# Optimization experiments

Measured on AMD Instinct MI355X. Metric: run time of the kernel, lower is better.

## Reference

```python
import jax, jax.numpy as jnp
import numpy as np
from jax.ops import segment_sum

IN_DIM, HID_DIM, OUT_DIM = 128, 128, 64
N_NODES, N_EDGES = 50000, 800000


def gcn_conv(x, src, dst, W, b, n_nodes):
    # Symmetric GCN normalization (no self loops): deg at targets from unit weights
    deg = segment_sum(jnp.ones(src.shape[0], dtype=x.dtype), dst, num_segments=n_nodes)
    dinv = jnp.where(deg > 0, jax.lax.rsqrt(jnp.maximum(deg, 1.0)), 0.0)
    norm = dinv[src] * dinv[dst]                      # [E]
    h = x @ W                                         # [N, out] small GEMM first (PyG order)
    msg = h[src] * norm[:, None]                      # gather + scale: [E, out]
    out = segment_sum(msg, dst, num_segments=n_nodes) # scatter-add to targets
    return out + b


def setup_inputs() -> dict:
    key = jax.random.key(0)
    k1, k2, k3, k4, k5 = jax.random.split(key, 5)
    x = jax.random.normal(k1, (N_NODES, IN_DIM), dtype=jnp.float32)
    edge_index = jax.random.randint(k2, (2, N_EDGES), 0, N_NODES, dtype=jnp.int64)
    s1 = 1.0 / np.sqrt(IN_DIM)
    s2 = 1.0 / np.sqrt(HID_DIM)
    W1 = jax.random.uniform(k3, (IN_DIM, HID_DIM), jnp.float32, -s1, s1)
    b1 = jnp.zeros((HID_DIM,), jnp.float32)
    W2 = jax.random.uniform(k4, (HID_DIM, OUT_DIM), jnp.float32, -s2, s2)
    b2 = jnp.zeros((OUT_DIM,), jnp.float32)
    return {"x": x, "edge_index": edge_index, "W1": W1, "b1": b1, "W2": W2, "b2": b2}


def reference(x, edge_index, W1, b1, W2, b2):
    n_nodes = x.shape[0]
    src, dst = edge_index[0], edge_index[1]
    h = gcn_conv(x, src, dst, W1, b1, n_nodes)
    h = jax.nn.relu(h)
    # Dropout is identity in eval mode (reference is deterministic)
    out = gcn_conv(h, src, dst, W2, b2, n_nodes)
    return out
```

## Files before the change

kernel.cpp:

```cpp
#include <hip/hip_runtime.h>

#define N_NODES 50000
#define N_EDGES 800000
#define IN_DIM  128
#define HID_DIM 128
#define OUT_DIM 64

#define NPAD 50176
#define CAP  64
#define GEMM1B ((N_NODES + 63) / 64)
#define FILLB (N_EDGES / 256)
#define W2PREPB 8

typedef __attribute__((ext_vector_type(8))) short bf16x8;
typedef __attribute__((ext_vector_type(4))) float f32x4;
typedef __attribute__((ext_vector_type(2))) float f32x2;

__device__ __forceinline__ unsigned short f2bf(float f) {
    unsigned u = __float_as_uint(f);
    u += 0x7fffu + ((u >> 16) & 1u);
    return (unsigned short)(u >> 16);
}
__device__ __forceinline__ float bflo(unsigned u) { return __uint_as_float(u << 16); }
__device__ __forceinline__ float bfhi(unsigned u) { return __uint_as_float(u & 0xffff0000u); }

#define ACC8(u)  do { \
    acc[0] += bflo(u.x); acc[1] += bfhi(u.x); \
    acc[2] += bflo(u.y); acc[3] += bfhi(u.y); \
    acc[4] += bflo(u.z); acc[5] += bfhi(u.z); \
    acc[6] += bflo(u.w); acc[7] += bfhi(u.w); } while (0)

__device__ __forceinline__ unsigned char f2fp8(float f) {
    return (unsigned char)(__builtin_amdgcn_cvt_pk_fp8_f32(f, f, 0, false) & 0xff);
}

#define ACCF8(u)  do { \
    f32x2 p0 = __builtin_amdgcn_cvt_pk_f32_fp8((int)u.x, false); \
    f32x2 p1 = __builtin_amdgcn_cvt_pk_f32_fp8((int)u.x, true);  \
    f32x2 p2 = __builtin_amdgcn_cvt_pk_f32_fp8((int)u.y, false); \
    f32x2 p3 = __builtin_amdgcn_cvt_pk_f32_fp8((int)u.y, true);  \
    acc[0] += p0[0]; acc[1] += p0[1]; \
    acc[2] += p1[0]; acc[3] += p1[1]; \
    acc[4] += p2[0]; acc[5] += p2[1]; \
    acc[6] += p3[0]; acc[7] += p3[1]; } while (0)

__device__ __forceinline__ float deg2dinv(int deg) {
    return (deg > 0) ? rsqrtf((float)deg) : 0.0f;
}

#define W1T_STRIDE 136


__global__ __launch_bounds__(256) void prep_fill_kernel(const int* __restrict__ src,
                                                        const int* __restrict__ dst,
                                                        int* __restrict__ cnt,
                                                        unsigned short* __restrict__ csr_src,
                                                        const float* __restrict__ W2,
                                                        unsigned short* __restrict__ w2t) {
    int bid = blockIdx.x;
    int tid = threadIdx.x;
    if (bid < W2PREPB) {
        int idx = bid * 256 + tid;
        int c = idx >> 5, k4 = (idx & 31) * 4;
        ushort4 o;
        o.x = f2bf(W2[(k4 + 0) * 64 + c]);
        o.y = f2bf(W2[(k4 + 1) * 64 + c]);
        o.z = f2bf(W2[(k4 + 2) * 64 + c]);
        o.w = f2bf(W2[(k4 + 3) * 64 + c]);
        *(ushort4*)(w2t + c * 128 + k4) = o;
    } else {
        int e = (bid - W2PREPB) * 256 + tid;
        int s = src[e], d = dst[e];
        int slot = atomicAdd(&cnt[d], 1);
        if (slot < CAP) csr_src[(d << 6) + slot] = (unsigned short)s;
    }
}


__global__ __launch_bounds__(256) void gemm1_kernel(const float* __restrict__ x,
                                                    const float* __restrict__ W1,
                                                    const int* __restrict__ cnt,
                                                    unsigned char* __restrict__ h1f8) {
    __shared__ unsigned short w1t[128 * W1T_STRIDE];

    int tid = threadIdx.x;
#pragma unroll
    for (int i = 0; i < 64; ++i) {
        int idx = i * 256 + tid;
        int k = idx >> 7, c = idx & 127;
        w1t[c * W1T_STRIDE + k] = f2bf(W1[idx]);
    }
    __syncthreads();

    int wave = tid >> 6;
    int lane = tid & 63;
    int n = lane & 15, quad = lane >> 4;
    int row0 = blockIdx.x * 64 + wave * 16;

    int arow = row0 + n;
    if (arow >= N_NODES) arow = N_NODES - 1;
    const float* aptr = x + (size_t)arow * 128 + quad * 8;
    const unsigned short* bbase = w1t + (size_t)n * W1T_STRIDE + quad * 8;

    f32x4 acc[8];
#pragma unroll
    for (int t = 0; t < 8; ++t) acc[t] = (f32x4){0.f, 0.f, 0.f, 0.f};

#pragma unroll
    for (int w4 = 0; w4 < 4; ++w4) {
        float4 f0 = *(const float4*)(aptr + w4 * 32);
        float4 f1 = *(const float4*)(aptr + w4 * 32 + 4);
        bf16x8 af;
        af[0] = (short)f2bf(f0.x); af[1] = (short)f2bf(f0.y);
        af[2] = (short)f2bf(f0.z); af[3] = (short)f2bf(f0.w);
        af[4] = (short)f2bf(f1.x); af[5] = (short)f2bf(f1.y);
        af[6] = (short)f2bf(f1.z); af[7] = (short)f2bf(f1.w);
#pragma unroll
        for (int t = 0; t < 8; ++t) {
            bf16x8 bf = *(const bf16x8*)(bbase + (size_t)t * 16 * W1T_STRIDE + w4 * 32);
            acc[t] = __builtin_amdgcn_mfma_f32_16x16x32_bf16(af, bf, acc[t], 0, 0, 0);
        }
    }

#pragma unroll
    for (int r = 0; r < 4; ++r) {
        int row = row0 + quad * 4 + r;
        if (row < N_NODES) {
            float dn = deg2dinv(cnt[row]);
            unsigned char* o = h1f8 + (size_t)row * 128 + n;
#pragma unroll
            for (int t = 0; t < 8; ++t) o[t * 16] = f2fp8(acc[t][r] * dn);
        }
    }
}


#define A1T_STRIDE 136

__global__ __launch_bounds__(256) void agg1_gemm2_fused(const unsigned short* __restrict__ csr_src,
                                                        const int* __restrict__ cnt,
                                                        const float* __restrict__ b1,
                                                        const unsigned char* __restrict__ h1f8,
                                                        const unsigned short* __restrict__ w2t,
                                                        unsigned short* __restrict__ h2b) {
    __shared__ unsigned short a1t[16 * A1T_STRIDE];

    int node0 = blockIdx.x * 16;
    int g = threadIdx.x >> 4;
    int q = threadIdx.x & 15;
    int node = node0 + g;
    int start = node << 6;
    int m = cnt[node];
    float dn = deg2dinv(m);
    if (m > CAP) m = CAP;

    float acc[8] = {};
    int j = 0;
    for (; j + 7 < m; j += 8) {
        ushort4 sa = *(const ushort4*)(csr_src + start + j);
        ushort4 sb = *(const ushort4*)(csr_src + start + j + 4);
        uint2 u0 = ((const uint2*)(h1f8 + (size_t)sa.x * 128))[q];
        uint2 u1 = ((const uint2*)(h1f8 + (size_t)sa.y * 128))[q];
        uint2 u2 = ((const uint2*)(h1f8 + (size_t)sa.z * 128))[q];
        uint2 u3 = ((const uint2*)(h1f8 + (size_t)sa.w * 128))[q];
        uint2 u4 = ((const uint2*)(h1f8 + (size_t)sb.x * 128))[q];
        uint2 u5 = ((const uint2*)(h1f8 + (size_t)sb.y * 128))[q];
        uint2 u6 = ((const uint2*)(h1f8 + (size_t)sb.z * 128))[q];
        uint2 u7 = ((const uint2*)(h1f8 + (size_t)sb.w * 128))[q];
        ACCF8(u0); ACCF8(u1); ACCF8(u2); ACCF8(u3);
        ACCF8(u4); ACCF8(u5); ACCF8(u6); ACCF8(u7);
    }
    for (; j + 3 < m; j += 4) {
        ushort4 sa = *(const ushort4*)(csr_src + start + j);
        uint2 u0 = ((const uint2*)(h1f8 + (size_t)sa.x * 128))[q];
        uint2 u1 = ((const uint2*)(h1f8 + (size_t)sa.y * 128))[q];
        uint2 u2 = ((const uint2*)(h1f8 + (size_t)sa.z * 128))[q];
        uint2 u3 = ((const uint2*)(h1f8 + (size_t)sa.w * 128))[q];
        ACCF8(u0); ACCF8(u1); ACCF8(u2); ACCF8(u3);
    }
    for (; j < m; ++j) {
        int s0 = csr_src[start + j];
        uint2 u0 = ((const uint2*)(h1f8 + (size_t)s0 * 128))[q];
        ACCF8(u0);
    }

    {
        float4 bA = ((const float4*)b1)[2 * q];
        float4 bB = ((const float4*)b1)[2 * q + 1];
        ushort4 oA, oB;
        oA.x = f2bf(fmaxf(acc[0] * dn + bA.x, 0.f));
        oA.y = f2bf(fmaxf(acc[1] * dn + bA.y, 0.f));
        oA.z = f2bf(fmaxf(acc[2] * dn + bA.z, 0.f));
        oA.w = f2bf(fmaxf(acc[3] * dn + bA.w, 0.f));
        oB.x = f2bf(fmaxf(acc[4] * dn + bB.x, 0.f));
        oB.y = f2bf(fmaxf(acc[5] * dn + bB.y, 0.f));
        oB.z = f2bf(fmaxf(acc[6] * dn + bB.z, 0.f));
        oB.w = f2bf(fmaxf(acc[7] * dn + bB.w, 0.f));
        ushort4* o = (ushort4*)(a1t + g * A1T_STRIDE + q * 8);
        o[0] = oA;
        o[1] = oB;
    }
    __syncthreads();

    int wave = threadIdx.x >> 6;
    int lane = threadIdx.x & 63;
    int n = lane & 15, quad = lane >> 4;
    const unsigned short* bbase = w2t + (size_t)(wave * 16 + n) * 128 + quad * 8;
    const unsigned short* abase = a1t + (size_t)n * A1T_STRIDE + quad * 8;

    f32x4 c2 = (f32x4){0.f, 0.f, 0.f, 0.f};
#pragma unroll
    for (int w4 = 0; w4 < 4; ++w4) {
        bf16x8 af = *(const bf16x8*)(abase + w4 * 32);
        bf16x8 bf = *(const bf16x8*)(bbase + w4 * 32);
        c2 = __builtin_amdgcn_mfma_f32_16x16x32_bf16(af, bf, c2, 0, 0, 0);
    }

#pragma unroll
    for (int r = 0; r < 4; ++r) {
        int row = node0 + quad * 4 + r;
        float dr = deg2dinv(cnt[row]);
        h2b[(size_t)row * 64 + wave * 16 + n] = f2bf(c2[r] * dr);
    }
}


__global__ __launch_bounds__(256) void agg2_kernel(const unsigned short* __restrict__ csr_src,
                                                   const int* __restrict__ cnt,
                                                   const float* __restrict__ b2,
                                                   const unsigned short* __restrict__ h2b,
                                                   float* __restrict__ out) {
    int node = blockIdx.x * 4 + (threadIdx.x >> 6);
    if (node >= N_NODES) return;
    int lane = threadIdx.x & 63;
    int grp = lane >> 3;
    int q   = lane & 7;
    int start = node << 6;
    int m = cnt[node];
    float dn = deg2dinv(m);
    if (m > CAP) m = CAP;

    float acc[8] = {};

    int j = grp;
    for (; j + 8 < m; j += 16) {
        int s0 = csr_src[start + j];
        int s1 = csr_src[start + j + 8];
        uint4 u0 = ((const uint4*)(h2b + (size_t)s0 * 64))[q];
        uint4 u1 = ((const uint4*)(h2b + (size_t)s1 * 64))[q];
        ACC8(u0); ACC8(u1);
    }
    if (j < m) {
        int s0 = csr_src[start + j];
        uint4 u0 = ((const uint4*)(h2b + (size_t)s0 * 64))[q];
        ACC8(u0);
    }

#pragma unroll
    for (int d = 8; d <= 32; d <<= 1) {
#pragma unroll
        for (int c = 0; c < 8; ++c) acc[c] += __shfl_xor(acc[c], d, 64);
    }

    if (lane < 8) {
        float4 bA = ((const float4*)b2)[2 * q];
        float4 bB = ((const float4*)b2)[2 * q + 1];
        float4 rA, rB;
        rA.x = acc[0] * dn + bA.x;
        rA.y = acc[1] * dn + bA.y;
        rA.z = acc[2] * dn + bA.z;
        rA.w = acc[3] * dn + bA.w;
        rB.x = acc[4] * dn + bB.x;
        rB.y = acc[5] * dn + bB.y;
        rB.z = acc[6] * dn + bB.z;
        rB.w = acc[7] * dn + bB.w;
        float4* o = (float4*)(out + (size_t)node * 64);
        o[2 * q] = rA;
        o[2 * q + 1] = rB;
    }
}


extern "C" void kernel_launch(void* const* d_in, const int* in_sizes, int n_in,
                              void* d_out, int out_size, void* d_ws, size_t ws_size,
                              hipStream_t stream) {
    const float* x  = (const float*)d_in[0];
    const int*   ei = (const int*)d_in[1];
    const float* W1 = (const float*)d_in[2];
    const float* b1 = (const float*)d_in[3];
    const float* W2 = (const float*)d_in[4];
    const float* b2 = (const float*)d_in[5];
    float* out = (float*)d_out;

    const int* src = ei;
    const int* dst = ei + N_EDGES;

    char* ws = (char*)d_ws;
    int*   cnt       = (int*)ws;
    unsigned short* csr_src = (unsigned short*)(cnt + NPAD);
    unsigned char* h1f8 = (unsigned char*)(csr_src + (size_t)N_NODES * CAP);
    unsigned short* h2b = (unsigned short*)(h1f8 + (size_t)N_NODES * HID_DIM);
    unsigned short* w2t = h2b + (size_t)N_NODES * OUT_DIM;

    (void)hipMemsetAsync(cnt, 0, NPAD * sizeof(int), stream);

    prep_fill_kernel<<<W2PREPB + FILLB, 256, 0, stream>>>(src, dst, cnt, csr_src,
                                                          W2, w2t);

    gemm1_kernel<<<GEMM1B, 256, 0, stream>>>(x, W1, cnt, h1f8);

    agg1_gemm2_fused<<<N_NODES / 16, 256, 0, stream>>>(csr_src, cnt, b1, h1f8, w2t, h2b);

    agg2_kernel<<<(N_NODES + 3) / 4, 256, 0, stream>>>(csr_src, cnt, b2, h2b, out);
}
```

Before: 179.6 us.

## Use one wave per node in agg1 with edge-parallel lanes and shuffle reduction

The layer-1 aggregation used to assign 16 threads to each node, with each thread walking every edge serially. It now uses a full wave per node: 8 lane groups take different edges, each lane reads 16 bytes of the fp8 row, and partial sums are combined with xor shuffles. Blocks grow to 1024 threads so that 16 nodes still fill the shared tile used by the fused MFMA GEMM, which only four waves execute. The aim is more memory-level parallelism on the gathers, paid for with shuffle-reduction overhead, idle waves during the GEMM, and larger blocks that may limit occupancy.

```diff
diff --git a/kernel.cpp b/kernel.cpp
--- a/kernel.cpp
+++ b/kernel.cpp
@@ -34,15 +34,19 @@
     return (unsigned char)(__builtin_amdgcn_cvt_pk_fp8_f32(f, f, 0, false) & 0xff);
 }
 
-#define ACCF8(u)  do { \
+#define ACCF16(u)  do { \
     f32x2 p0 = __builtin_amdgcn_cvt_pk_f32_fp8((int)u.x, false); \
     f32x2 p1 = __builtin_amdgcn_cvt_pk_f32_fp8((int)u.x, true);  \
     f32x2 p2 = __builtin_amdgcn_cvt_pk_f32_fp8((int)u.y, false); \
     f32x2 p3 = __builtin_amdgcn_cvt_pk_f32_fp8((int)u.y, true);  \
-    acc[0] += p0[0]; acc[1] += p0[1]; \
-    acc[2] += p1[0]; acc[3] += p1[1]; \
-    acc[4] += p2[0]; acc[5] += p2[1]; \
-    acc[6] += p3[0]; acc[7] += p3[1]; } while (0)
+    f32x2 p4 = __builtin_amdgcn_cvt_pk_f32_fp8((int)u.z, false); \
+    f32x2 p5 = __builtin_amdgcn_cvt_pk_f32_fp8((int)u.z, true);  \
+    f32x2 p6 = __builtin_amdgcn_cvt_pk_f32_fp8((int)u.w, false); \
+    f32x2 p7 = __builtin_amdgcn_cvt_pk_f32_fp8((int)u.w, true);  \
+    acc[0]  += p0[0]; acc[1]  += p0[1]; acc[2]  += p1[0]; acc[3]  += p1[1]; \
+    acc[4]  += p2[0]; acc[5]  += p2[1]; acc[6]  += p3[0]; acc[7]  += p3[1]; \
+    acc[8]  += p4[0]; acc[9]  += p4[1]; acc[10] += p5[0]; acc[11] += p5[1]; \
+    acc[12] += p6[0]; acc[13] += p6[1]; acc[14] += p7[0]; acc[15] += p7[1]; } while (0)
 
 __device__ __forceinline__ float deg2dinv(int deg) {
     return (deg > 0) ? rsqrtf((float)deg) : 0.0f;
@@ -137,90 +141,93 @@
 
 #define A1T_STRIDE 136
 
-__global__ __launch_bounds__(256) void agg1_gemm2_fused(const unsigned short* __restrict__ csr_src,
-                                                        const int* __restrict__ cnt,
-                                                        const float* __restrict__ b1,
-                                                        const unsigned char* __restrict__ h1f8,
-                                                        const unsigned short* __restrict__ w2t,
-                                                        unsigned short* __restrict__ h2b) {
+__global__ __launch_bounds__(1024) void agg1_gemm2_fused(const unsigned short* __restrict__ csr_src,
+                                                         const int* __restrict__ cnt,
+                                                         const float* __restrict__ b1,
+                                                         const unsigned char* __restrict__ h1f8,
+                                                         const unsigned short* __restrict__ w2t,
+                                                         unsigned short* __restrict__ h2b) {
     __shared__ unsigned short a1t[16 * A1T_STRIDE];
 
     int node0 = blockIdx.x * 16;
-    int g = threadIdx.x >> 4;
-    int q = threadIdx.x & 15;
-    int node = node0 + g;
+    int wave = threadIdx.x >> 6;
+    int lane = threadIdx.x & 63;
+    int grp = lane >> 3;
+    int q   = lane & 7;
+    int node = node0 + wave;
     int start = node << 6;
     int m = cnt[node];
     float dn = deg2dinv(m);
     if (m > CAP) m = CAP;
 
-    float acc[8] = {};
-    int j = 0;
-    for (; j + 7 < m; j += 8) {
-        ushort4 sa = *(const ushort4*)(csr_src + start + j);
-        ushort4 sb = *(const ushort4*)(csr_src + start + j + 4);
-        uint2 u0 = ((const uint2*)(h1f8 + (size_t)sa.x * 128))[q];
-        uint2 u1 = ((const uint2*)(h1f8 + (size_t)sa.y * 128))[q];
-        uint2 u2 = ((const uint2*)(h1f8 + (size_t)sa.z * 128))[q];
-        uint2 u3 = ((const uint2*)(h1f8 + (size_t)sa.w * 128))[q];
-        uint2 u4 = ((const uint2*)(h1f8 + (size_t)sb.x * 128))[q];
-        uint2 u5 = ((const uint2*)(h1f8 + (size_t)sb.y * 128))[q];
-        uint2 u6 = ((const uint2*)(h1f8 + (size_t)sb.z * 128))[q];
-        uint2 u7 = ((const uint2*)(h1f8 + (size_t)sb.w * 128))[q];
-        ACCF8(u0); ACCF8(u1); ACCF8(u2); ACCF8(u3);
-        ACCF8(u4); ACCF8(u5); ACCF8(u6); ACCF8(u7);
-    }
-    for (; j + 3 < m; j += 4) {
-        ushort4 sa = *(const ushort4*)(csr_src + start + j);
-        uint2 u0 = ((const uint2*)(h1f8 + (size_t)sa.x * 128))[q];
-        uint2 u1 = ((const uint2*)(h1f8 + (size_t)sa.y * 128))[q];
-        uint2 u2 = ((const uint2*)(h1f8 + (size_t)sa.z * 128))[q];
-        uint2 u3 = ((const uint2*)(h1f8 + (size_t)sa.w * 128))[q];
-        ACCF8(u0); ACCF8(u1); ACCF8(u2); ACCF8(u3);
-    }
-    for (; j < m; ++j) {
+    float acc[16] = {};
+    int j = grp;
+    for (; j + 8 < m; j += 16) {
         int s0 = csr_src[start + j];
-        uint2 u0 = ((const uint2*)(h1f8 + (size_t)s0 * 128))[q];
-        ACCF8(u0);
-    }
-
-    {
-        float4 bA = ((const float4*)b1)[2 * q];
-        float4 bB = ((const float4*)b1)[2 * q + 1];
-        ushort4 oA, oB;
-        oA.x = f2bf(fmaxf(acc[0] * dn + bA.x, 0.f));
-        oA.y = f2bf(fmaxf(acc[1] * dn + bA.y, 0.f));
-        oA.z = f2bf(fmaxf(acc[2] * dn + bA.z, 0.f));
-        oA.w = f2bf(fmaxf(acc[3] * dn + bA.w, 0.f));
-        oB.x = f2bf(fmaxf(acc[4] * dn + bB.x, 0.f));
-        oB.y = f2bf(fmaxf(acc[5] * dn + bB.y, 0.f));
-        oB.z = f2bf(fmaxf(acc[6] * dn + bB.z, 0.f));
-        oB.w = f2bf(fmaxf(acc[7] * dn + bB.w, 0.f));
-        ushort4* o = (ushort4*)(a1t + g * A1T_STRIDE + q * 8);
-        o[0] = oA;
-        o[1] = oB;
+        int s1 = csr_src[start + j + 8];
+        uint4 u0 = ((const uint4*)(h1f8 + (size_t)s0 * 128))[q];
+        uint4 u1 = ((const uint4*)(h1f8 + (size_t)s1 * 128))[q];
+        ACCF16(u0); ACCF16(u1);
+    }
+    if (j < m) {
+        int s0 = csr_src[start + j];
+        uint4 u0 = ((const uint4*)(h1f8 + (size_t)s0 * 128))[q];
+        ACCF16(u0);
+    }
+
+#pragma unroll
+    for (int d = 8; d <= 32; d <<= 1) {
+#pragma unroll
+        for (int c = 0; c < 16; ++c) acc[c] += __shfl_xor(acc[c], d, 64);
+    }
+
+    if (grp == 0) {
+        int c0 = q * 16;
+        float4 bA = *(const float4*)(b1 + c0);
+        float4 bB = *(const float4*)(b1 + c0 + 4);
+        float4 bC = *(const float4*)(b1 + c0 + 8);
+        float4 bD = *(const float4*)(b1 + c0 + 12);
+        ushort4 oA, oB, oC, oD;
+        oA.x = f2bf(fmaxf(acc[0]  * dn + bA.x, 0.f));
+        oA.y = f2bf(fmaxf(acc[1]  * dn + bA.y, 0.f));
+        oA.z = f2bf(fmaxf(acc[2]  * dn + bA.z, 0.f));
+        oA.w = f2bf(fmaxf(acc[3]  * dn + bA.w, 0.f));
+        oB.x = f2bf(fmaxf(acc[4]  * dn + bB.x, 0.f));
+        oB.y = f2bf(fmaxf(acc[5]  * dn + bB.y, 0.f));
+        oB.z = f2bf(fmaxf(acc[6]  * dn + bB.z, 0.f));
+        oB.w = f2bf(fmaxf(acc[7]  * dn + bB.w, 0.f));
+        oC.x = f2bf(fmaxf(acc[8]  * dn + bC.x, 0.f));
+        oC.y = f2bf(fmaxf(acc[9]  * dn + bC.y, 0.f));
+        oC.z = f2bf(fmaxf(acc[10] * dn + bC.z, 0.f));
+        oC.w = f2bf(fmaxf(acc[11] * dn + bC.w, 0.f));
+        oD.x = f2bf(fmaxf(acc[12] * dn + bD.x, 0.f));
+        oD.y = f2bf(fmaxf(acc[13] * dn + bD.y, 0.f));
+        oD.z = f2bf(fmaxf(acc[14] * dn + bD.z, 0.f));
+        oD.w = f2bf(fmaxf(acc[15] * dn + bD.w, 0.f));
+        ushort4* o = (ushort4*)(a1t + wave * A1T_STRIDE + c0);
+        o[0] = oA; o[1] = oB; o[2] = oC; o[3] = oD;
     }
     __syncthreads();
 
-    int wave = threadIdx.x >> 6;
-    int lane = threadIdx.x & 63;
-    int n = lane & 15, quad = lane >> 4;
-    const unsigned short* bbase = w2t + (size_t)(wave * 16 + n) * 128 + quad * 8;
-    const unsigned short* abase = a1t + (size_t)n * A1T_STRIDE + quad * 8;
-
-    f32x4 c2 = (f32x4){0.f, 0.f, 0.f, 0.f};
-#pragma unroll
-    for (int w4 = 0; w4 < 4; ++w4) {
-        bf16x8 af = *(const bf16x8*)(abase + w4 * 32);
-        bf16x8 bf = *(const bf16x8*)(bbase + w4 * 32);
-        c2 = __builtin_amdgcn_mfma_f32_16x16x32_bf16(af, bf, c2, 0, 0, 0);
-    }
-
-#pragma unroll
-    for (int r = 0; r < 4; ++r) {
-        int row = node0 + quad * 4 + r;
-        float dr = deg2dinv(cnt[row]);
-        h2b[(size_t)row * 64 + wave * 16 + n] = f2bf(c2[r] * dr);
+    if (wave < 4) {
+        int n = lane & 15, quad = lane >> 4;
+        const unsigned short* bbase = w2t + (size_t)(wave * 16 + n) * 128 + quad * 8;
+        const unsigned short* abase = a1t + (size_t)n * A1T_STRIDE + quad * 8;
+
+        f32x4 c2 = (f32x4){0.f, 0.f, 0.f, 0.f};
+#pragma unroll
+        for (int w4 = 0; w4 < 4; ++w4) {
+            bf16x8 af = *(const bf16x8*)(abase + w4 * 32);
+            bf16x8 bf = *(const bf16x8*)(bbase + w4 * 32);
+            c2 = __builtin_amdgcn_mfma_f32_16x16x32_bf16(af, bf, c2, 0, 0, 0);
+        }
+
+#pragma unroll
+        for (int r = 0; r < 4; ++r) {
+            int row = node0 + quad * 4 + r;
+            float dr = deg2dinv(cnt[row]);
+            h2b[(size_t)row * 64 + wave * 16 + n] = f2bf(c2[r] * dr);
+        }
     }
 }
 
@@ -309,7 +316,7 @@
 
     gemm1_kernel<<<GEMM1B, 256, 0, stream>>>(x, W1, cnt, h1f8);
 
-    agg1_gemm2_fused<<<N_NODES / 16, 256, 0, stream>>>(csr_src, cnt, b1, h1f8, w2t, h2b);
+    agg1_gemm2_fused<<<N_NODES / 16, 1024, 0, stream>>>(csr_src, cnt, b1, h1f8, w2t, h2b);
 
     agg2_kernel<<<(N_NODES + 3) / 4, 256, 0, stream>>>(csr_src, cnt, b2, h2b, out);
 }
```

Result: slower. 199.3 us (+11.0%).
